# Optimization experiments

Measured on AMD Instinct MI355X. Metric: run time of the kernel, lower is better.

The kernel has to match this reference:

```python
import jax, jax.numpy as jnp
import numpy as np

STATE_DIM = 4096
HIDDEN_DIM = 4096
GRU_STEP = 8
N_NODES = 4


def setup_inputs() -> dict:
    key = jax.random.key(0)
    ks = jax.random.split(key, 8)
    s = STATE_DIM
    scale = 0.02  # keep gate pre-activations in a sane range
    return {
        "A_out": jax.random.uniform(ks[0], (N_NODES, N_NODES), dtype=jnp.float32),
        "A_in": jax.random.uniform(ks[1], (N_NODES, N_NODES), dtype=jnp.float32),
        "annotation": jax.random.normal(ks[2], (N_NODES, s), dtype=jnp.float32),
        "W_ih": jax.random.normal(ks[3], (3 * s, 2 * s), dtype=jnp.float32) * scale,
        "W_hh": jax.random.normal(ks[4], (3 * s, s), dtype=jnp.float32) * scale,
        "fc1_w": jax.random.normal(ks[5], (HIDDEN_DIM, N_NODES * s), dtype=jnp.float32) * scale,
        "fc1_b": jnp.zeros((HIDDEN_DIM,), dtype=jnp.float32),
        "fc2_w": jax.random.normal(ks[6], (2, HIDDEN_DIM), dtype=jnp.float32) * scale,
        "fc2_b": jnp.zeros((2,), dtype=jnp.float32),
    }


def _gru_cell(x, h, W_ih, W_hh):
    # PyTorch GRUCell (bias=False), gate order r, z, n
    gi = x @ W_ih.T  # [N, 3*s]
    gh = h @ W_hh.T  # [N, 3*s]
    i_r, i_z, i_n = jnp.split(gi, 3, axis=1)
    h_r, h_z, h_n = jnp.split(gh, 3, axis=1)
    r = jax.nn.sigmoid(i_r + h_r)
    z = jax.nn.sigmoid(i_z + h_z)
    n = jnp.tanh(i_n + r * h_n)
    return (1.0 - z) * n + z * h


def reference(A_out, A_in, annotation, W_ih, W_hh, fc1_w, fc1_b, fc2_w, fc2_b):
    def step(h, _):
        a = jnp.concatenate((A_out @ h, A_in @ h), axis=1)  # [N, 2*s]
        return _gru_cell(a, h, W_ih, W_hh), None

    h, _ = jax.lax.scan(step, annotation, None, length=GRU_STEP)
    enc = h.reshape(1, -1)  # [1, N*s]
    x = enc @ fc1_w.T + fc1_b
    x = x @ fc2_w.T + fc2_b
    return jax.nn.log_softmax(x, axis=1)
```

## Files before the change

### kernel.cpp

```cpp
#include <hip/hip_runtime.h>
#include <hip/hip_bf16.h>
#include <math.h>


#define S 4096

__device__ __forceinline__ float wave_reduce_add(float v) {
#pragma unroll
    for (int off = 32; off > 0; off >>= 1) v += __shfl_down(v, off, 64);
    return v;
}

__global__ void init_h_k(const float* __restrict__ ann, float4* __restrict__ h) {
    int k = blockIdx.x * 256 + threadIdx.x;
    float4 o;
    o.x = ann[k];
    o.y = ann[S + k];
    o.z = ann[2 * S + k];
    o.w = ann[3 * S + k];
    h[k] = o;
}

__global__ void compute_a_k(const float* __restrict__ Aout, const float* __restrict__ Ain,
                            const float4* __restrict__ h, float4* __restrict__ a) {
    int k = blockIdx.x * 256 + threadIdx.x;
    const float* M = (k < S) ? Aout : Ain;
    int kk = k & (S - 1);
    float4 hv = h[kk];
    float4 o;
    o.x = M[0]  * hv.x + M[1]  * hv.y + M[2]  * hv.z + M[3]  * hv.w;
    o.y = M[4]  * hv.x + M[5]  * hv.y + M[6]  * hv.z + M[7]  * hv.w;
    o.z = M[8]  * hv.x + M[9]  * hv.y + M[10] * hv.z + M[11] * hv.w;
    o.w = M[12] * hv.x + M[13] * hv.y + M[14] * hv.z + M[15] * hv.w;
    a[k] = o;
}

__global__ __launch_bounds__(256) void gru_col_k(
    const float* __restrict__ Wih, const float* __restrict__ Whh,
    const float4* __restrict__ a, const float4* __restrict__ hcur,
    float4* __restrict__ hnext) {
    const int c = blockIdx.x;
    const int t = threadIdx.x;

    float accI[3][4];
    float accH[3][4];
#pragma unroll
    for (int g = 0; g < 3; g++)
#pragma unroll
        for (int n = 0; n < 4; n++) { accI[g][n] = 0.f; accH[g][n] = 0.f; }

    const float4* Wi[3];
    Wi[0] = (const float4*)(Wih + (size_t)(0 * S + c) * (2 * S));
    Wi[1] = (const float4*)(Wih + (size_t)(1 * S + c) * (2 * S));
    Wi[2] = (const float4*)(Wih + (size_t)(2 * S + c) * (2 * S));

#pragma unroll 2
    for (int i = 0; i < 8; i++) {
        int j = t + 256 * i;
        int ka = 4 * j;
        float4 a0 = a[ka + 0];
        float4 a1 = a[ka + 1];
        float4 a2 = a[ka + 2];
        float4 a3 = a[ka + 3];
#pragma unroll
        for (int g = 0; g < 3; g++) {
            float4 w = Wi[g][j];
            accI[g][0] += w.x * a0.x + w.y * a1.x + w.z * a2.x + w.w * a3.x;
            accI[g][1] += w.x * a0.y + w.y * a1.y + w.z * a2.y + w.w * a3.y;
            accI[g][2] += w.x * a0.z + w.y * a1.z + w.z * a2.z + w.w * a3.z;
            accI[g][3] += w.x * a0.w + w.y * a1.w + w.z * a2.w + w.w * a3.w;
        }
    }

    const float4* Wh[3];
    Wh[0] = (const float4*)(Whh + (size_t)(0 * S + c) * S);
    Wh[1] = (const float4*)(Whh + (size_t)(1 * S + c) * S);
    Wh[2] = (const float4*)(Whh + (size_t)(2 * S + c) * S);

#pragma unroll 2
    for (int i = 0; i < 4; i++) {
        int j = t + 256 * i;
        int ka = 4 * j;
        float4 h0 = hcur[ka + 0];
        float4 h1 = hcur[ka + 1];
        float4 h2 = hcur[ka + 2];
        float4 h3 = hcur[ka + 3];
#pragma unroll
        for (int g = 0; g < 3; g++) {
            float4 w = Wh[g][j];
            accH[g][0] += w.x * h0.x + w.y * h1.x + w.z * h2.x + w.w * h3.x;
            accH[g][1] += w.x * h0.y + w.y * h1.y + w.z * h2.y + w.w * h3.y;
            accH[g][2] += w.x * h0.z + w.y * h1.z + w.z * h2.z + w.w * h3.z;
            accH[g][3] += w.x * h0.w + w.y * h1.w + w.z * h2.w + w.w * h3.w;
        }
    }

    __shared__ float red[4][24];
    int lane = t & 63, wid = t >> 6;
#pragma unroll
    for (int g = 0; g < 3; g++) {
#pragma unroll
        for (int n = 0; n < 4; n++) {
            float vI = wave_reduce_add(accI[g][n]);
            float vH = wave_reduce_add(accH[g][n]);
            if (lane == 0) {
                red[wid][g * 4 + n] = vI;
                red[wid][12 + g * 4 + n] = vH;
            }
        }
    }
    __syncthreads();

    if (t < 4) {
        int n = t;
        float I[3], H[3];
#pragma unroll
        for (int g = 0; g < 3; g++) {
            I[g] = red[0][g * 4 + n] + red[1][g * 4 + n] + red[2][g * 4 + n] + red[3][g * 4 + n];
            H[g] = red[0][12 + g * 4 + n] + red[1][12 + g * 4 + n] + red[2][12 + g * 4 + n] + red[3][12 + g * 4 + n];
        }
        float r = 1.f / (1.f + expf(-(I[0] + H[0])));
        float z = 1.f / (1.f + expf(-(I[1] + H[1])));
        float nn = tanhf(I[2] + r * H[2]);
        float hv = ((const float*)hcur)[c * 4 + n];
        ((float*)hnext)[c * 4 + n] = (1.f - z) * nn + z * hv;
    }
}

__global__ void enc_k(const float4* __restrict__ h, float* __restrict__ enc) {
    int idx = blockIdx.x * 256 + threadIdx.x;
    int n = idx >> 12;
    int k = idx & (S - 1);
    enc[idx] = ((const float*)h)[k * 4 + n];
}

__global__ __launch_bounds__(256) void fc1_k(const float* __restrict__ W, const float* __restrict__ b,
                                             const float* __restrict__ enc, float* __restrict__ x1) {
    int j = blockIdx.x, t = threadIdx.x;
    const float4* row = (const float4*)(W + (size_t)j * (4 * S));
    const float4* e4 = (const float4*)enc;
    float acc = 0.f;
#pragma unroll 4
    for (int i = 0; i < 16; i++) {
        int m = t + 256 * i;
        float4 w = row[m];
        float4 e = e4[m];
        acc += w.x * e.x + w.y * e.y + w.z * e.z + w.w * e.w;
    }
    acc = wave_reduce_add(acc);
    __shared__ float red[4];
    if ((t & 63) == 0) red[t >> 6] = acc;
    __syncthreads();
    if (t == 0) x1[j] = red[0] + red[1] + red[2] + red[3] + b[j];
}

__global__ __launch_bounds__(256) void fc2_k(const float* __restrict__ W, const float* __restrict__ b,
                                             const float* __restrict__ x1, float* __restrict__ out) {
    int t = threadIdx.x;
    const float4* x4 = (const float4*)x1;
    const float4* w0 = (const float4*)W;
    const float4* w1 = (const float4*)(W + S);
    float a0 = 0.f, a1 = 0.f;
#pragma unroll
    for (int i = 0; i < 4; i++) {
        int m = t + 256 * i;
        float4 x = x4[m];
        float4 u = w0[m];
        float4 v = w1[m];
        a0 += u.x * x.x + u.y * x.y + u.z * x.z + u.w * x.w;
        a1 += v.x * x.x + v.y * x.y + v.z * x.z + v.w * x.w;
    }
    a0 = wave_reduce_add(a0);
    a1 = wave_reduce_add(a1);
    __shared__ float red0[4], red1[4];
    int lane = t & 63, wid = t >> 6;
    if (lane == 0) { red0[wid] = a0; red1[wid] = a1; }
    __syncthreads();
    if (t == 0) {
        float l0 = red0[0] + red0[1] + red0[2] + red0[3] + b[0];
        float l1 = red1[0] + red1[1] + red1[2] + red1[3] + b[1];
        float m = fmaxf(l0, l1);
        float ls = m + logf(expf(l0 - m) + expf(l1 - m));
        out[0] = l0 - ls;
        out[1] = l1 - ls;
    }
}

extern "C" void kernel_launch(void* const* d_in, const int* in_sizes, int n_in,
                              void* d_out, int out_size, void* d_ws, size_t ws_size,
                              hipStream_t stream) {
    const float* A_out = (const float*)d_in[0];
    const float* A_in  = (const float*)d_in[1];
    const float* ann   = (const float*)d_in[2];
    const float* W_ih  = (const float*)d_in[3];
    const float* W_hh  = (const float*)d_in[4];
    const float* fc1_w = (const float*)d_in[5];
    const float* fc1_b = (const float*)d_in[6];
    const float* fc2_w = (const float*)d_in[7];
    const float* fc2_b = (const float*)d_in[8];
    float* out = (float*)d_out;

    float* ws_f = (float*)d_ws;
    float4* hA  = (float4*)ws_f;
    float4* hB  = hA + S;
    float4* a_t = hB + S;
    float* enc  = (float*)(a_t + 2 * S);
    float* x1   = enc + 4 * S;

    init_h_k<<<S / 256, 256, 0, stream>>>(ann, hA);

    for (int step = 0; step < 8; step++) {
        float4* cur = (step & 1) ? hB : hA;
        float4* nxt = (step & 1) ? hA : hB;
        compute_a_k<<<2 * S / 256, 256, 0, stream>>>(A_out, A_in, cur, a_t);
        gru_col_k<<<S, 256, 0, stream>>>(W_ih, W_hh, a_t, cur, nxt);
    }
    enc_k<<<4 * S / 256, 256, 0, stream>>>(hA, enc);
    fc1_k<<<S, 256, 0, stream>>>(fc1_w, fc1_b, enc, x1);
    fc2_k<<<1, 256, 0, stream>>>(fc2_w, fc2_b, x1, out);
}
```

Measured before the change: 1.679 ms.

## Fuse adjacency mixing into GRU kernel and merge input/hidden weight loops

Removes the separate compute_a_k kernel: each GRU block now loads the 4x4 A_out/A_in matrices into registers and computes the aggregated input on the fly from h, instead of reading a precomputed a buffer. The input-weight and hidden-weight loops are merged into one loop that issues nine weight vector loads per iteration. This cuts eight kernel launches and the a-buffer write/read traffic, and gives more loads in flight per iteration. In exchange each block redundantly recomputes the small matrix-vector products, and register pressure rises.

```diff
diff --git a/kernel.cpp b/kernel.cpp
--- a/kernel.cpp
+++ b/kernel.cpp
@@ -1,9 +1,10 @@
 #include <hip/hip_runtime.h>
-#include <hip/hip_bf16.h>
 #include <math.h>
 
 
 #define S 4096
+
+typedef float f4 __attribute__((ext_vector_type(4)));
 
 __device__ __forceinline__ float wave_reduce_add(float v) {
 #pragma unroll
@@ -11,9 +12,25 @@
     return v;
 }
 
-__global__ void init_h_k(const float* __restrict__ ann, float4* __restrict__ h) {
+__device__ __forceinline__ f4 mv4(const float* A, f4 h) {
+    f4 r;
+    r.x = A[0]  * h.x + A[1]  * h.y + A[2]  * h.z + A[3]  * h.w;
+    r.y = A[4]  * h.x + A[5]  * h.y + A[6]  * h.z + A[7]  * h.w;
+    r.z = A[8]  * h.x + A[9]  * h.y + A[10] * h.z + A[11] * h.w;
+    r.w = A[12] * h.x + A[13] * h.y + A[14] * h.z + A[15] * h.w;
+    return r;
+}
+
+__device__ __forceinline__ void acc4(float* acc, f4 w, f4 v0, f4 v1, f4 v2, f4 v3) {
+    acc[0] += w.x * v0.x + w.y * v1.x + w.z * v2.x + w.w * v3.x;
+    acc[1] += w.x * v0.y + w.y * v1.y + w.z * v2.y + w.w * v3.y;
+    acc[2] += w.x * v0.z + w.y * v1.z + w.z * v2.z + w.w * v3.z;
+    acc[3] += w.x * v0.w + w.y * v1.w + w.z * v2.w + w.w * v3.w;
+}
+
+__global__ void init_h_k(const float* __restrict__ ann, f4* __restrict__ h) {
     int k = blockIdx.x * 256 + threadIdx.x;
-    float4 o;
+    f4 o;
     o.x = ann[k];
     o.y = ann[S + k];
     o.z = ann[2 * S + k];
@@ -21,27 +38,17 @@
     h[k] = o;
 }
 
-__global__ void compute_a_k(const float* __restrict__ Aout, const float* __restrict__ Ain,
-                            const float4* __restrict__ h, float4* __restrict__ a) {
-    int k = blockIdx.x * 256 + threadIdx.x;
-    const float* M = (k < S) ? Aout : Ain;
-    int kk = k & (S - 1);
-    float4 hv = h[kk];
-    float4 o;
-    o.x = M[0]  * hv.x + M[1]  * hv.y + M[2]  * hv.z + M[3]  * hv.w;
-    o.y = M[4]  * hv.x + M[5]  * hv.y + M[6]  * hv.z + M[7]  * hv.w;
-    o.z = M[8]  * hv.x + M[9]  * hv.y + M[10] * hv.z + M[11] * hv.w;
-    o.w = M[12] * hv.x + M[13] * hv.y + M[14] * hv.z + M[15] * hv.w;
-    a[k] = o;
-}
-
-__global__ __launch_bounds__(256) void gru_col_k(
+__global__ __launch_bounds__(256) void gru_fused_k(
     const float* __restrict__ Wih, const float* __restrict__ Whh,
-    const float4* __restrict__ a, const float4* __restrict__ hcur,
-    float4* __restrict__ hnext) {
+    const float* __restrict__ Aout, const float* __restrict__ Ain,
+    const f4* __restrict__ hcur, f4* __restrict__ hnext) {
     const int c = blockIdx.x;
     const int t = threadIdx.x;
 
+    float AO[16], AI[16];
+#pragma unroll
+    for (int q = 0; q < 16; q++) { AO[q] = Aout[q]; AI[q] = Ain[q]; }
+
     float accI[3][4];
     float accH[3][4];
 #pragma unroll
@@ -49,50 +56,51 @@
 #pragma unroll
         for (int n = 0; n < 4; n++) { accI[g][n] = 0.f; accH[g][n] = 0.f; }
 
-    const float4* Wi[3];
-    Wi[0] = (const float4*)(Wih + (size_t)(0 * S + c) * (2 * S));
-    Wi[1] = (const float4*)(Wih + (size_t)(1 * S + c) * (2 * S));
-    Wi[2] = (const float4*)(Wih + (size_t)(2 * S + c) * (2 * S));
-
-#pragma unroll 2
-    for (int i = 0; i < 8; i++) {
-        int j = t + 256 * i;
-        int ka = 4 * j;
-        float4 a0 = a[ka + 0];
-        float4 a1 = a[ka + 1];
-        float4 a2 = a[ka + 2];
-        float4 a3 = a[ka + 3];
-#pragma unroll
-        for (int g = 0; g < 3; g++) {
-            float4 w = Wi[g][j];
-            accI[g][0] += w.x * a0.x + w.y * a1.x + w.z * a2.x + w.w * a3.x;
-            accI[g][1] += w.x * a0.y + w.y * a1.y + w.z * a2.y + w.w * a3.y;
-            accI[g][2] += w.x * a0.z + w.y * a1.z + w.z * a2.z + w.w * a3.z;
-            accI[g][3] += w.x * a0.w + w.y * a1.w + w.z * a2.w + w.w * a3.w;
-        }
-    }
-
-    const float4* Wh[3];
-    Wh[0] = (const float4*)(Whh + (size_t)(0 * S + c) * S);
-    Wh[1] = (const float4*)(Whh + (size_t)(1 * S + c) * S);
-    Wh[2] = (const float4*)(Whh + (size_t)(2 * S + c) * S);
+    const f4* wi0 = (const f4*)(Wih + (size_t)(0 * S + c) * (2 * S));
+    const f4* wi1 = (const f4*)(Wih + (size_t)(1 * S + c) * (2 * S));
+    const f4* wi2 = (const f4*)(Wih + (size_t)(2 * S + c) * (2 * S));
+    const f4* wh0 = (const f4*)(Whh + (size_t)(0 * S + c) * S);
+    const f4* wh1 = (const f4*)(Whh + (size_t)(1 * S + c) * S);
+    const f4* wh2 = (const f4*)(Whh + (size_t)(2 * S + c) * S);
 
 #pragma unroll 2
     for (int i = 0; i < 4; i++) {
         int j = t + 256 * i;
-        int ka = 4 * j;
-        float4 h0 = hcur[ka + 0];
-        float4 h1 = hcur[ka + 1];
-        float4 h2 = hcur[ka + 2];
-        float4 h3 = hcur[ka + 3];
-#pragma unroll
-        for (int g = 0; g < 3; g++) {
-            float4 w = Wh[g][j];
-            accH[g][0] += w.x * h0.x + w.y * h1.x + w.z * h2.x + w.w * h3.x;
-            accH[g][1] += w.x * h0.y + w.y * h1.y + w.z * h2.y + w.w * h3.y;
-            accH[g][2] += w.x * h0.z + w.y * h1.z + w.z * h2.z + w.w * h3.z;
-            accH[g][3] += w.x * h0.w + w.y * h1.w + w.z * h2.w + w.w * h3.w;
-        }
+        int kh = 4 * j;
+        f4 h0 = hcur[kh + 0];
+        f4 h1 = hcur[kh + 1];
+        f4 h2 = hcur[kh + 2];
+        f4 h3 = hcur[kh + 3];
+
+        f4 wA0 = wi0[j];
+        f4 wA1 = wi1[j];
+        f4 wA2 = wi2[j];
+        f4 wB0 = wi0[j + 1024];
+        f4 wB1 = wi1[j + 1024];
+        f4 wB2 = wi2[j + 1024];
+        f4 wC0 = wh0[j];
+        f4 wC1 = wh1[j];
+        f4 wC2 = wh2[j];
+
+        f4 a0 = mv4(AO, h0);
+        f4 a1 = mv4(AO, h1);
+        f4 a2 = mv4(AO, h2);
+        f4 a3 = mv4(AO, h3);
+        acc4(accI[0], wA0, a0, a1, a2, a3);
+        acc4(accI[1], wA1, a0, a1, a2, a3);
+        acc4(accI[2], wA2, a0, a1, a2, a3);
+
+        a0 = mv4(AI, h0);
+        a1 = mv4(AI, h1);
+        a2 = mv4(AI, h2);
+        a3 = mv4(AI, h3);
+        acc4(accI[0], wB0, a0, a1, a2, a3);
+        acc4(accI[1], wB1, a0, a1, a2, a3);
+        acc4(accI[2], wB2, a0, a1, a2, a3);
+
+        acc4(accH[0], wC0, h0, h1, h2, h3);
+        acc4(accH[1], wC1, h0, h1, h2, h3);
+        acc4(accH[2], wC2, h0, h1, h2, h3);
     }
 
     __shared__ float red[4][24];
@@ -127,7 +135,7 @@
     }
 }
 
-__global__ void enc_k(const float4* __restrict__ h, float* __restrict__ enc) {
+__global__ void enc_k(const f4* __restrict__ h, float* __restrict__ enc) {
     int idx = blockIdx.x * 256 + threadIdx.x;
     int n = idx >> 12;
     int k = idx & (S - 1);
@@ -137,14 +145,14 @@
 __global__ __launch_bounds__(256) void fc1_k(const float* __restrict__ W, const float* __restrict__ b,
                                              const float* __restrict__ enc, float* __restrict__ x1) {
     int j = blockIdx.x, t = threadIdx.x;
-    const float4* row = (const float4*)(W + (size_t)j * (4 * S));
-    const float4* e4 = (const float4*)enc;
+    const f4* row = (const f4*)(W + (size_t)j * (4 * S));
+    const f4* e4 = (const f4*)enc;
     float acc = 0.f;
 #pragma unroll 4
     for (int i = 0; i < 16; i++) {
         int m = t + 256 * i;
-        float4 w = row[m];
-        float4 e = e4[m];
+        f4 w = row[m];
+        f4 e = e4[m];
         acc += w.x * e.x + w.y * e.y + w.z * e.z + w.w * e.w;
     }
     acc = wave_reduce_add(acc);
@@ -157,16 +165,16 @@
 __global__ __launch_bounds__(256) void fc2_k(const float* __restrict__ W, const float* __restrict__ b,
                                              const float* __restrict__ x1, float* __restrict__ out) {
     int t = threadIdx.x;
-    const float4* x4 = (const float4*)x1;
-    const float4* w0 = (const float4*)W;
-    const float4* w1 = (const float4*)(W + S);
+    const f4* x4 = (const f4*)x1;
+    const f4* w0 = (const f4*)W;
+    const f4* w1 = (const f4*)(W + S);
     float a0 = 0.f, a1 = 0.f;
 #pragma unroll
     for (int i = 0; i < 4; i++) {
         int m = t + 256 * i;
-        float4 x = x4[m];
-        float4 u = w0[m];
-        float4 v = w1[m];
+        f4 x = x4[m];
+        f4 u = w0[m];
+        f4 v = w1[m];
         a0 += u.x * x.x + u.y * x.y + u.z * x.z + u.w * x.w;
         a1 += v.x * x.x + v.y * x.y + v.z * x.z + v.w * x.w;
     }
@@ -201,19 +209,17 @@
     float* out = (float*)d_out;
 
     float* ws_f = (float*)d_ws;
-    float4* hA  = (float4*)ws_f;
-    float4* hB  = hA + S;
-    float4* a_t = hB + S;
-    float* enc  = (float*)(a_t + 2 * S);
-    float* x1   = enc + 4 * S;
+    f4* hA  = (f4*)ws_f;
+    f4* hB  = hA + S;
+    float* enc = (float*)(hB + S);
+    float* x1  = enc + 4 * S;
 
     init_h_k<<<S / 256, 256, 0, stream>>>(ann, hA);
 
     for (int step = 0; step < 8; step++) {
-        float4* cur = (step & 1) ? hB : hA;
-        float4* nxt = (step & 1) ? hA : hB;
-        compute_a_k<<<2 * S / 256, 256, 0, stream>>>(A_out, A_in, cur, a_t);
-        gru_col_k<<<S, 256, 0, stream>>>(W_ih, W_hh, a_t, cur, nxt);
+        f4* cur = (step & 1) ? hB : hA;
+        f4* nxt = (step & 1) ? hA : hB;
+        gru_fused_k<<<S, 256, 0, stream>>>(W_ih, W_hh, A_out, A_in, cur, nxt);
     }
     enc_k<<<4 * S / 256, 256, 0, stream>>>(hA, enc);
     fc1_k<<<S, 256, 0, stream>>>(fc1_w, fc1_b, enc, x1);
```

Result: no change. 1.695 ms (+1.0%).
